# Performance work log

Hardware: AMD Instinct MI355X
Metric: run time of the kernel (lower is better)

The kernel has to match this reference:

```python
import jax, jax.numpy as jnp
import numpy as np

D_MODEL = 2048
R = 32
LN_EPS = 1e-5  # torch nn.LayerNorm default


def setup_inputs() -> dict:
    key = jax.random.key(0)
    k_x, k_wd, k_wu = jax.random.split(key, 3)
    x = jax.random.normal(k_x, (4, 4096, D_MODEL), dtype=jnp.float32)
    gamma = jnp.ones((D_MODEL,), dtype=jnp.float32)
    beta = jnp.zeros((D_MODEL,), dtype=jnp.float32)
    # down: default torch Linear init ~ U(-1/sqrt(d), 1/sqrt(d)); approximate with scaled normal
    w_down = jax.random.normal(k_wd, (D_MODEL, R), dtype=jnp.float32) / jnp.sqrt(jnp.float32(D_MODEL))
    b_down = jnp.zeros((R,), dtype=jnp.float32)
    # up: nn.init.normal_(std=0.001), bias zero
    w_up = jax.random.normal(k_wu, (R, D_MODEL), dtype=jnp.float32) * 0.001
    b_up = jnp.zeros((D_MODEL,), dtype=jnp.float32)
    return {"x": x, "gamma": gamma, "beta": beta, "w_down": w_down,
            "b_down": b_down, "w_up": w_up, "b_up": b_up}


def reference(x, gamma, beta, w_down, b_down, w_up, b_up):
    # LayerNorm over last dim
    mu = jnp.mean(x, axis=-1, keepdims=True)
    var = jnp.mean(jnp.square(x - mu), axis=-1, keepdims=True)
    h = (x - mu) * jax.lax.rsqrt(var + LN_EPS) * gamma + beta
    # down-proj -> exact GELU (torch nn.GELU default) -> up-proj -> residual
    h = jnp.einsum('bsd,dr->bsr', h, w_down) + b_down
    h = jax.nn.gelu(h, approximate=False)
    h = jnp.einsum('bsr,rd->bsd', h, w_up) + b_up
    return x + h
```

## Files before the change

### kernel.cpp

```cpp
#include <hip/hip_runtime.h>
#include <math.h>

#define D     2048
#define NR    32
#define ROWS  8
#define JP    68
#define XRW   (32 * JP)

__device__ __forceinline__ void fma4(float a, const float4& w, float4& o) {
    o.x = fmaf(a, w.x, o.x);
    o.y = fmaf(a, w.y, o.y);
    o.z = fmaf(a, w.z, o.z);
    o.w = fmaf(a, w.w, o.w);
}

__device__ __forceinline__ float wred(float v) {
    #pragma unroll
    for (int off = 32; off >= 1; off >>= 1) v += __shfl_xor(v, off);
    return v;
}

__global__ __launch_bounds__(256)
void k_prep(const float* __restrict__ wd, const float* __restrict__ gamma,
            const float* __restrict__ beta, float* __restrict__ wdp,
            float* __restrict__ c12p)
{
    __shared__ float red[4][64];
    const int tid = threadIdx.x;
    const int l = tid & 63, w = tid >> 6;
    const int j = blockIdx.x * 256 + tid;

    const float gv = gamma[j], bv = beta[j];
    float4 c1a[8], c2a[8];
    #pragma unroll
    for (int q = 0; q < 8; ++q) {
        float4 wv = *(const float4*)(wd + j * NR + q * 4);
        float4 wp = make_float4(gv * wv.x, gv * wv.y, gv * wv.z, gv * wv.w);
        *(float4*)(wdp + j * NR + q * 4) = wp;
        c1a[q] = wp;
        c2a[q] = make_float4(bv * wv.x, bv * wv.y, bv * wv.z, bv * wv.w);
    }
    #pragma unroll
    for (int q = 0; q < 8; ++q) {
        c1a[q].x = wred(c1a[q].x); c1a[q].y = wred(c1a[q].y);
        c1a[q].z = wred(c1a[q].z); c1a[q].w = wred(c1a[q].w);
        c2a[q].x = wred(c2a[q].x); c2a[q].y = wred(c2a[q].y);
        c2a[q].z = wred(c2a[q].z); c2a[q].w = wred(c2a[q].w);
    }
    if (l == 0) {
        #pragma unroll
        for (int q = 0; q < 8; ++q) {
            red[w][q * 4 + 0] = c1a[q].x; red[w][q * 4 + 1] = c1a[q].y;
            red[w][q * 4 + 2] = c1a[q].z; red[w][q * 4 + 3] = c1a[q].w;
            red[w][32 + q * 4 + 0] = c2a[q].x; red[w][32 + q * 4 + 1] = c2a[q].y;
            red[w][32 + q * 4 + 2] = c2a[q].z; red[w][32 + q * 4 + 3] = c2a[q].w;
        }
    }
    __syncthreads();
    if (tid < 64)
        c12p[blockIdx.x * 64 + tid] = red[0][tid] + red[1][tid] + red[2][tid] + red[3][tid];
}

__global__ __launch_bounds__(256, 2)
void k_fused(const float* __restrict__ x, const float* __restrict__ bd,
             const float* __restrict__ wu, const float* __restrict__ bu,
             const float* __restrict__ wdp, const float* __restrict__ c12p,
             float* __restrict__ out)
{
    __shared__ float xs[ROWS * XRW];
    __shared__ float S4[4][ROWS][NR];
    __shared__ float a_s[ROWS][NR];
    __shared__ float mu_s[ROWS], rs_s[ROWS];
    __shared__ float c1s[NR], c2s[NR], bds[NR];

    const int tid = threadIdx.x;
    const int w = tid >> 6, l = tid & 63;
    const long row0 = (long)blockIdx.x * ROWS;

    if (tid < NR) {
        float a1 = 0.f, a2 = 0.f;
        #pragma unroll
        for (int p = 0; p < 8; ++p) {
            a1 += c12p[p * 64 + tid];
            a2 += c12p[p * 64 + 32 + tid];
        }
        c1s[tid] = a1; c2s[tid] = a2; bds[tid] = bd[tid];
    }

    #pragma unroll
    for (int rp = 0; rp < 2; ++rp) {
        const int row = w * 2 + rp;
        const float* xr = x + (row0 + row) * D;
        float s = 0.f, s2 = 0.f;
        #pragma unroll
        for (int it = 0; it < 8; ++it) {
            const int j = it * 256 + l * 4;
            float4 v = *(const float4*)(xr + j);
            *(float4*)&xs[row * XRW + (j >> 6) * JP + (j & 63)] = v;
            s  += v.x + v.y + v.z + v.w;
            s2 += v.x * v.x + v.y * v.y + v.z * v.z + v.w * v.w;
        }
        #pragma unroll
        for (int off = 32; off >= 1; off >>= 1) {
            s  += __shfl_xor(s, off);
            s2 += __shfl_xor(s2, off);
        }
        if (l == 0) {
            const float mu  = s * (1.0f / D);
            const float var = s2 * (1.0f / D) - mu * mu;
            mu_s[row] = mu;
            rs_s[row] = rsqrtf(var + 1e-5f);
        }
    }
    __syncthreads();

    {
        const int rg = tid & 7, r0 = rg * 4, jo = tid >> 3;
        float4 acc[ROWS];
        #pragma unroll
        for (int m = 0; m < ROWS; ++m) acc[m] = make_float4(0.f, 0.f, 0.f, 0.f);

        const float* wp_base = wdp + (jo * 64) * NR + r0;
        #pragma unroll 4
        for (int tq = 0; tq < 16; ++tq) {
            const float4 w0 = *(const float4*)(wp_base + (tq * 4 + 0) * NR);
            const float4 w1 = *(const float4*)(wp_base + (tq * 4 + 1) * NR);
            const float4 w2 = *(const float4*)(wp_base + (tq * 4 + 2) * NR);
            const float4 w3 = *(const float4*)(wp_base + (tq * 4 + 3) * NR);
            #pragma unroll
            for (int m = 0; m < ROWS; ++m) {
                const float4 xv = *(const float4*)&xs[m * XRW + jo * JP + tq * 4];
                fma4(xv.x, w0, acc[m]);
                fma4(xv.y, w1, acc[m]);
                fma4(xv.z, w2, acc[m]);
                fma4(xv.w, w3, acc[m]);
            }
        }
        #pragma unroll
        for (int m = 0; m < ROWS; ++m) {
            #pragma unroll
            for (int off = 8; off <= 32; off <<= 1) {
                acc[m].x += __shfl_xor(acc[m].x, off);
                acc[m].y += __shfl_xor(acc[m].y, off);
                acc[m].z += __shfl_xor(acc[m].z, off);
                acc[m].w += __shfl_xor(acc[m].w, off);
            }
        }
        if (l < 8) {
            #pragma unroll
            for (int m = 0; m < ROWS; ++m)
                *(float4*)&S4[w][m][l * 4] = acc[m];
        }
    }
    __syncthreads();

    {
        const int m = tid >> 5, r = tid & 31;
        const float S = S4[0][m][r] + S4[1][m][r] + S4[2][m][r] + S4[3][m][r];
        const float y = rs_s[m] * (S - mu_s[m] * c1s[r]) + c2s[r] + bds[r];
        a_s[m][r] = 0.5f * y * (1.0f + erff(y * 0.70710678118654752f));
    }
    __syncthreads();

    #pragma unroll 1
    for (int c = 0; c < 2; ++c) {
        const int j  = c * 1024 + tid * 4;
        const int xo = (j >> 6) * JP + (j & 63);
        const float4 bv = *(const float4*)(bu + j);
        float4 o[ROWS];
        #pragma unroll
        for (int m = 0; m < ROWS; ++m) {
            const float4 xv = *(const float4*)&xs[m * XRW + xo];
            o[m] = make_float4(xv.x + bv.x, xv.y + bv.y, xv.z + bv.z, xv.w + bv.w);
        }
        #pragma unroll 4
        for (int rq = 0; rq < 8; ++rq) {
            float4 ar[ROWS];
            #pragma unroll
            for (int m = 0; m < ROWS; ++m)
                ar[m] = *(const float4*)&a_s[m][rq * 4];
            #pragma unroll
            for (int rr = 0; rr < 4; ++rr) {
                const float4 wv = *(const float4*)(wu + (rq * 4 + rr) * D + j);
                #pragma unroll
                for (int m = 0; m < ROWS; ++m) {
                    const float av = (rr == 0) ? ar[m].x : (rr == 1) ? ar[m].y
                                   : (rr == 2) ? ar[m].z : ar[m].w;
                    fma4(av, wv, o[m]);
                }
            }
        }
        #pragma unroll
        for (int m = 0; m < ROWS; ++m) {
            float* op = out + (row0 + m) * D + j;
            __builtin_nontemporal_store(o[m].x, op + 0);
            __builtin_nontemporal_store(o[m].y, op + 1);
            __builtin_nontemporal_store(o[m].z, op + 2);
            __builtin_nontemporal_store(o[m].w, op + 3);
        }
    }
}

extern "C" void kernel_launch(void* const* d_in, const int* in_sizes, int n_in,
                              void* d_out, int out_size, void* d_ws, size_t ws_size,
                              hipStream_t stream) {
    (void)n_in; (void)ws_size; (void)out_size;
    const float* x     = (const float*)d_in[0];
    const float* gamma = (const float*)d_in[1];
    const float* beta  = (const float*)d_in[2];
    const float* wd    = (const float*)d_in[3];
    const float* bd    = (const float*)d_in[4];
    const float* wu    = (const float*)d_in[5];
    const float* bu    = (const float*)d_in[6];
    float* out  = (float*)d_out;
    float* wdp  = (float*)d_ws;
    float* c12p = wdp + D * NR;

    const int nrows  = in_sizes[0] / D;
    const int blocks = nrows / ROWS;

    hipLaunchKernelGGL(k_prep,  dim3(8),      dim3(256), 0, stream, wd, gamma, beta, wdp, c12p);
    hipLaunchKernelGGL(k_fused, dim3(blocks), dim3(256), 0, stream, x, bd, wu, bu, wdp, c12p, out);
}
```

Before: 283.3 us.

## Store x tile as bf16 in LDS and reload fp32 x from global for residual

The LDS copy of the x tile is now packed as bf16 pairs, which halves shared memory per block, and launch bounds are raised to allow four blocks per CU. The down-projection dot product reads the bf16 values, while the residual add re-reads full-precision x from global memory (likely an L2 hit). This trades a second global read and bf16 rounding in the down-projection for higher occupancy. The bf16 error is scaled by the small up-projection weights, so accuracy risk is modest.

Result: slower. 305.5 us (+7.8%).

```diff
diff --git a/kernel.cpp b/kernel.cpp
--- a/kernel.cpp
+++ b/kernel.cpp
@@ -4,8 +4,15 @@
 #define D     2048
 #define NR    32
 #define ROWS  8
-#define JP    68
-#define XRW   (32 * JP)
+#define CU    34
+#define XRU   (32 * CU)
+
+__device__ __forceinline__ unsigned int f2bf(float f) {
+    unsigned int u = __float_as_uint(f);
+    return (u + 0x7FFFu + ((u >> 16) & 1u)) >> 16;
+}
+__device__ __forceinline__ float bflo(unsigned int p) { return __uint_as_float(p << 16); }
+__device__ __forceinline__ float bfhi(unsigned int p) { return __uint_as_float(p & 0xFFFF0000u); }
 
 __device__ __forceinline__ void fma4(float a, const float4& w, float4& o) {
     o.x = fmaf(a, w.x, o.x);
@@ -61,13 +68,13 @@
         c12p[blockIdx.x * 64 + tid] = red[0][tid] + red[1][tid] + red[2][tid] + red[3][tid];
 }
 
-__global__ __launch_bounds__(256, 2)
+__global__ __launch_bounds__(256, 4)
 void k_fused(const float* __restrict__ x, const float* __restrict__ bd,
              const float* __restrict__ wu, const float* __restrict__ bu,
              const float* __restrict__ wdp, const float* __restrict__ c12p,
              float* __restrict__ out)
 {
-    __shared__ float xs[ROWS * XRW];
+    __shared__ unsigned int xs[ROWS * XRU];
     __shared__ float S4[4][ROWS][NR];
     __shared__ float a_s[ROWS][NR];
     __shared__ float mu_s[ROWS], rs_s[ROWS];
@@ -96,7 +103,10 @@
         for (int it = 0; it < 8; ++it) {
             const int j = it * 256 + l * 4;
             float4 v = *(const float4*)(xr + j);
-            *(float4*)&xs[row * XRW + (j >> 6) * JP + (j & 63)] = v;
+            uint2 p;
+            p.x = f2bf(v.x) | (f2bf(v.y) << 16);
+            p.y = f2bf(v.z) | (f2bf(v.w) << 16);
+            *(uint2*)&xs[row * XRU + (j >> 6) * CU + ((j & 63) >> 1)] = p;
             s  += v.x + v.y + v.z + v.w;
             s2 += v.x * v.x + v.y * v.y + v.z * v.z + v.w * v.w;
         }
@@ -121,6 +131,7 @@
         for (int m = 0; m < ROWS; ++m) acc[m] = make_float4(0.f, 0.f, 0.f, 0.f);
 
         const float* wp_base = wdp + (jo * 64) * NR + r0;
+        const unsigned int* xb = xs + jo * CU;
         #pragma unroll 4
         for (int tq = 0; tq < 16; ++tq) {
             const float4 w0 = *(const float4*)(wp_base + (tq * 4 + 0) * NR);
@@ -129,11 +140,11 @@
             const float4 w3 = *(const float4*)(wp_base + (tq * 4 + 3) * NR);
             #pragma unroll
             for (int m = 0; m < ROWS; ++m) {
-                const float4 xv = *(const float4*)&xs[m * XRW + jo * JP + tq * 4];
-                fma4(xv.x, w0, acc[m]);
-                fma4(xv.y, w1, acc[m]);
-                fma4(xv.z, w2, acc[m]);
-                fma4(xv.w, w3, acc[m]);
+                const uint2 hp = *(const uint2*)&xb[m * XRU + tq * 2];
+                fma4(bflo(hp.x), w0, acc[m]);
+                fma4(bfhi(hp.x), w1, acc[m]);
+                fma4(bflo(hp.y), w2, acc[m]);
+                fma4(bfhi(hp.y), w3, acc[m]);
             }
         }
         #pragma unroll
@@ -164,13 +175,12 @@
 
     #pragma unroll 1
     for (int c = 0; c < 2; ++c) {
-        const int j  = c * 1024 + tid * 4;
-        const int xo = (j >> 6) * JP + (j & 63);
+        const int j = c * 1024 + tid * 4;
         const float4 bv = *(const float4*)(bu + j);
         float4 o[ROWS];
         #pragma unroll
         for (int m = 0; m < ROWS; ++m) {
-            const float4 xv = *(const float4*)&xs[m * XRW + xo];
+            const float4 xv = *(const float4*)(x + (row0 + m) * D + j);
             o[m] = make_float4(xv.x + bv.x, xv.y + bv.y, xv.z + bv.z, xv.w + bv.w);
         }
         #pragma unroll 4
```

## Use bf16 MFMA for down and up projections with swizzled LDS and pre-packed weights

Applied to the files above, without the earlier changes.

Replaces the fp32 FMA loops for both low-rank projections with 16x16x32 bf16 MFMA instructions. x is stored in LDS as bf16 with an XOR swizzle, and both weight matrices are pre-packed into the MFMA fragment layout by a prep kernel. A small extra kernel reduces the LayerNorm-folding constants. The residual pass now re-reads x from global memory instead of LDS, and bf16 rounding of the activations and weights lowers the projection precision. Shared-memory use drops, so occupancy can rise to 4 blocks per SM, but only 8 of the 16 MFMA rows are used.

Result: no change. 287.5 us (+1.5%).

```diff
diff --git a/kernel.cpp b/kernel.cpp
--- a/kernel.cpp
+++ b/kernel.cpp
@@ -4,88 +4,91 @@
 #define D     2048
 #define NR    32
 #define ROWS  8
-#define JP    68
-#define XRW   (32 * JP)
-
-__device__ __forceinline__ void fma4(float a, const float4& w, float4& o) {
-    o.x = fmaf(a, w.x, o.x);
-    o.y = fmaf(a, w.y, o.y);
-    o.z = fmaf(a, w.z, o.z);
-    o.w = fmaf(a, w.w, o.w);
-}
-
-__device__ __forceinline__ float wred(float v) {
-    #pragma unroll
-    for (int off = 32; off >= 1; off >>= 1) v += __shfl_xor(v, off);
-    return v;
-}
-
-__global__ __launch_bounds__(256)
+
+typedef short bf16x8 __attribute__((ext_vector_type(8)));
+typedef float f32x4  __attribute__((ext_vector_type(4)));
+
+__device__ __forceinline__ unsigned int f2bf(float f) {
+    unsigned int u = __float_as_uint(f);
+    return (u + 0x7FFFu + ((u >> 16) & 1u)) >> 16;
+}
+__device__ __forceinline__ unsigned int pk2(float a, float b) {
+    return f2bf(a) | (f2bf(b) << 16);
+}
+
+__global__ __launch_bounds__(64)
 void k_prep(const float* __restrict__ wd, const float* __restrict__ gamma,
-            const float* __restrict__ beta, float* __restrict__ wdp,
+            const float* __restrict__ beta, const float* __restrict__ wu,
+            unsigned int* __restrict__ wuf, unsigned int* __restrict__ wdpf,
             float* __restrict__ c12p)
 {
-    __shared__ float red[4][64];
-    const int tid = threadIdx.x;
-    const int l = tid & 63, w = tid >> 6;
-    const int j = blockIdx.x * 256 + tid;
-
-    const float gv = gamma[j], bv = beta[j];
-    float4 c1a[8], c2a[8];
-    #pragma unroll
-    for (int q = 0; q < 8; ++q) {
-        float4 wv = *(const float4*)(wd + j * NR + q * 4);
-        float4 wp = make_float4(gv * wv.x, gv * wv.y, gv * wv.z, gv * wv.w);
-        *(float4*)(wdp + j * NR + q * 4) = wp;
-        c1a[q] = wp;
-        c2a[q] = make_float4(bv * wv.x, bv * wv.y, bv * wv.z, bv * wv.w);
-    }
-    #pragma unroll
-    for (int q = 0; q < 8; ++q) {
-        c1a[q].x = wred(c1a[q].x); c1a[q].y = wred(c1a[q].y);
-        c1a[q].z = wred(c1a[q].z); c1a[q].w = wred(c1a[q].w);
-        c2a[q].x = wred(c2a[q].x); c2a[q].y = wred(c2a[q].y);
-        c2a[q].z = wred(c2a[q].z); c2a[q].w = wred(c2a[q].w);
-    }
-    if (l == 0) {
-        #pragma unroll
-        for (int q = 0; q < 8; ++q) {
-            red[w][q * 4 + 0] = c1a[q].x; red[w][q * 4 + 1] = c1a[q].y;
-            red[w][q * 4 + 2] = c1a[q].z; red[w][q * 4 + 3] = c1a[q].w;
-            red[w][32 + q * 4 + 0] = c2a[q].x; red[w][32 + q * 4 + 1] = c2a[q].y;
-            red[w][32 + q * 4 + 2] = c2a[q].z; red[w][32 + q * 4 + 3] = c2a[q].w;
-        }
-    }
-    __syncthreads();
-    if (tid < 64)
-        c12p[blockIdx.x * 64 + tid] = red[0][tid] + red[1][tid] + red[2][tid] + red[3][tid];
-}
-
-__global__ __launch_bounds__(256, 2)
+    const int l = threadIdx.x;
+    const int q = l >> 4, p = l & 15;
+    const int b = blockIdx.x;
+    if (b < 128) {
+        const int t = b;
+        float v[8];
+        #pragma unroll
+        for (int e = 0; e < 8; ++e)
+            v[e] = wu[(q * 8 + e) * D + t * 16 + p];
+        uint4 pk;
+        pk.x = pk2(v[0], v[1]); pk.y = pk2(v[2], v[3]);
+        pk.z = pk2(v[4], v[5]); pk.w = pk2(v[6], v[7]);
+        *(uint4*)&wuf[(t * 64 + l) * 4] = pk;
+    } else {
+        const int idx = b - 128;
+        const int kk = idx >> 1, n = idx & 1;
+        const int r = n * 16 + p;
+        float wv[8];
+        float c1 = 0.f, c2 = 0.f;
+        #pragma unroll
+        for (int e = 0; e < 8; ++e) {
+            const int k = kk * 32 + q * 8 + e;
+            const float wdv = wd[k * NR + r];
+            wv[e] = gamma[k] * wdv;
+            c1 += wv[e];
+            c2 += beta[k] * wdv;
+        }
+        uint4 pk;
+        pk.x = pk2(wv[0], wv[1]); pk.y = pk2(wv[2], wv[3]);
+        pk.z = pk2(wv[4], wv[5]); pk.w = pk2(wv[6], wv[7]);
+        *(uint4*)&wdpf[(idx * 64 + l) * 4] = pk;
+        c1 += __shfl_xor(c1, 16); c1 += __shfl_xor(c1, 32);
+        c2 += __shfl_xor(c2, 16); c2 += __shfl_xor(c2, 32);
+        if (q == 0) {
+            c12p[idx * 32 + p]      = c1;
+            c12p[idx * 32 + 16 + p] = c2;
+        }
+    }
+}
+
+__global__ __launch_bounds__(64)
+void k_c12(const float* __restrict__ c12p, float* __restrict__ c12)
+{
+    const int i = threadIdx.x;
+    const int half = i >> 5, r = i & 31;
+    const int n = r >> 4, rr = r & 15;
+    float s = 0.f;
+    for (int kk = 0; kk < 64; ++kk)
+        s += c12p[(kk * 2 + n) * 32 + half * 16 + rr];
+    c12[i] = s;
+}
+
+__global__ __launch_bounds__(256, 4)
 void k_fused(const float* __restrict__ x, const float* __restrict__ bd,
-             const float* __restrict__ wu, const float* __restrict__ bu,
-             const float* __restrict__ wdp, const float* __restrict__ c12p,
+             const float* __restrict__ bu, const unsigned int* __restrict__ wuf,
+             const unsigned int* __restrict__ wdpf, const float* __restrict__ c12,
              float* __restrict__ out)
 {
-    __shared__ float xs[ROWS * XRW];
-    __shared__ float S4[4][ROWS][NR];
-    __shared__ float a_s[ROWS][NR];
+    __shared__ unsigned int xs[ROWS * 1024];
+    __shared__ float Sp[4][2][16][8];
+    __shared__ unsigned short a_sh[ROWS][NR];
     __shared__ float mu_s[ROWS], rs_s[ROWS];
-    __shared__ float c1s[NR], c2s[NR], bds[NR];
 
     const int tid = threadIdx.x;
     const int w = tid >> 6, l = tid & 63;
+    const int p = l & 15, q = l >> 4;
     const long row0 = (long)blockIdx.x * ROWS;
-
-    if (tid < NR) {
-        float a1 = 0.f, a2 = 0.f;
-        #pragma unroll
-        for (int p = 0; p < 8; ++p) {
-            a1 += c12p[p * 64 + tid];
-            a2 += c12p[p * 64 + 32 + tid];
-        }
-        c1s[tid] = a1; c2s[tid] = a2; bds[tid] = bd[tid];
-    }
 
     #pragma unroll
     for (int rp = 0; rp < 2; ++rp) {
@@ -96,7 +99,11 @@
         for (int it = 0; it < 8; ++it) {
             const int j = it * 256 + l * 4;
             float4 v = *(const float4*)(xr + j);
-            *(float4*)&xs[row * XRW + (j >> 6) * JP + (j & 63)] = v;
+            uint2 pkk;
+            pkk.x = pk2(v.x, v.y);
+            pkk.y = pk2(v.z, v.w);
+            const int byte = (row * 4096 + j * 2) ^ (row << 4);
+            *(uint2*)((char*)xs + byte) = pkk;
             s  += v.x + v.y + v.z + v.w;
             s2 += v.x * v.x + v.y * v.y + v.z * v.z + v.w * v.w;
         }
@@ -115,88 +122,60 @@
     __syncthreads();
 
     {
-        const int rg = tid & 7, r0 = rg * 4, jo = tid >> 3;
-        float4 acc[ROWS];
-        #pragma unroll
-        for (int m = 0; m < ROWS; ++m) acc[m] = make_float4(0.f, 0.f, 0.f, 0.f);
-
-        const float* wp_base = wdp + (jo * 64) * NR + r0;
+        f32x4 acc0 = {0.f, 0.f, 0.f, 0.f}, acc1 = {0.f, 0.f, 0.f, 0.f};
+        const bool arow = p < ROWS;
         #pragma unroll 4
-        for (int tq = 0; tq < 16; ++tq) {
-            const float4 w0 = *(const float4*)(wp_base + (tq * 4 + 0) * NR);
-            const float4 w1 = *(const float4*)(wp_base + (tq * 4 + 1) * NR);
-            const float4 w2 = *(const float4*)(wp_base + (tq * 4 + 2) * NR);
-            const float4 w3 = *(const float4*)(wp_base + (tq * 4 + 3) * NR);
-            #pragma unroll
-            for (int m = 0; m < ROWS; ++m) {
-                const float4 xv = *(const float4*)&xs[m * XRW + jo * JP + tq * 4];
-                fma4(xv.x, w0, acc[m]);
-                fma4(xv.y, w1, acc[m]);
-                fma4(xv.z, w2, acc[m]);
-                fma4(xv.w, w3, acc[m]);
+        for (int t = 0; t < 16; ++t) {
+            bf16x8 af = {0, 0, 0, 0, 0, 0, 0, 0};
+            if (arow) {
+                const int byte = (p * 4096 + (w * 512 + t * 32) * 2 + q * 16) ^ (p << 4);
+                af = *(const bf16x8*)((const char*)xs + byte);
             }
-        }
-        #pragma unroll
-        for (int m = 0; m < ROWS; ++m) {
-            #pragma unroll
-            for (int off = 8; off <= 32; off <<= 1) {
-                acc[m].x += __shfl_xor(acc[m].x, off);
-                acc[m].y += __shfl_xor(acc[m].y, off);
-                acc[m].z += __shfl_xor(acc[m].z, off);
-                acc[m].w += __shfl_xor(acc[m].w, off);
-            }
-        }
-        if (l < 8) {
-            #pragma unroll
-            for (int m = 0; m < ROWS; ++m)
-                *(float4*)&S4[w][m][l * 4] = acc[m];
+            const int base = (w * 16 + t) * 512 + l * 4;
+            const bf16x8 b0 = *(const bf16x8*)&wdpf[base];
+            const bf16x8 b1 = *(const bf16x8*)&wdpf[base + 256];
+            acc0 = __builtin_amdgcn_mfma_f32_16x16x32_bf16(af, b0, acc0, 0, 0, 0);
+            acc1 = __builtin_amdgcn_mfma_f32_16x16x32_bf16(af, b1, acc1, 0, 0, 0);
+        }
+        if (l < 32) {
+            *(f32x4*)&Sp[w][0][p][(q & 1) * 4] = acc0;
+            *(f32x4*)&Sp[w][1][p][(q & 1) * 4] = acc1;
         }
     }
     __syncthreads();
 
     {
         const int m = tid >> 5, r = tid & 31;
-        const float S = S4[0][m][r] + S4[1][m][r] + S4[2][m][r] + S4[3][m][r];
-        const float y = rs_s[m] * (S - mu_s[m] * c1s[r]) + c2s[r] + bds[r];
-        a_s[m][r] = 0.5f * y * (1.0f + erff(y * 0.70710678118654752f));
+        const int n = r >> 4, rr = r & 15;
+        const float S = Sp[0][n][rr][m] + Sp[1][n][rr][m]
+                      + Sp[2][n][rr][m] + Sp[3][n][rr][m];
+        const float y = rs_s[m] * (S - mu_s[m] * c12[r]) + c12[32 + r] + bd[r];
+        const float a = 0.5f * y * (1.0f + erff(y * 0.70710678118654752f));
+        a_sh[m][r] = (unsigned short)f2bf(a);
     }
     __syncthreads();
 
-    #pragma unroll 1
-    for (int c = 0; c < 2; ++c) {
-        const int j  = c * 1024 + tid * 4;
-        const int xo = (j >> 6) * JP + (j & 63);
-        const float4 bv = *(const float4*)(bu + j);
-        float4 o[ROWS];
-        #pragma unroll
-        for (int m = 0; m < ROWS; ++m) {
-            const float4 xv = *(const float4*)&xs[m * XRW + xo];
-            o[m] = make_float4(xv.x + bv.x, xv.y + bv.y, xv.z + bv.z, xv.w + bv.w);
-        }
+    {
+        bf16x8 afc = {0, 0, 0, 0, 0, 0, 0, 0};
+        if (p < ROWS) afc = *(const bf16x8*)((const char*)a_sh + p * 64 + q * 16);
+        const bool act = p < ROWS;
+        const long xbase = (row0 + p) * D;
+        const f32x4 z = {0.f, 0.f, 0.f, 0.f};
         #pragma unroll 4
-        for (int rq = 0; rq < 8; ++rq) {
-            float4 ar[ROWS];
-            #pragma unroll
-            for (int m = 0; m < ROWS; ++m)
-                ar[m] = *(const float4*)&a_s[m][rq * 4];
-            #pragma unroll
-            for (int rr = 0; rr < 4; ++rr) {
-                const float4 wv = *(const float4*)(wu + (rq * 4 + rr) * D + j);
-                #pragma unroll
-                for (int m = 0; m < ROWS; ++m) {
-                    const float av = (rr == 0) ? ar[m].x : (rr == 1) ? ar[m].y
-                                   : (rr == 2) ? ar[m].z : ar[m].w;
-                    fma4(av, wv, o[m]);
-                }
+        for (int t = 0; t < 32; ++t) {
+            const int j0 = w * 512 + t * 16;
+            const bf16x8 bw = *(const bf16x8*)&wuf[(j0 >> 4) * 256 + l * 4];
+            f32x4 dd = __builtin_amdgcn_mfma_f32_16x16x32_bf16(bw, afc, z, 0, 0, 0);
+            if (act) {
+                const int jj = j0 + q * 4;
+                const float4 xv = *(const float4*)(x + xbase + jj);
+                const float4 bv = *(const float4*)(bu + jj);
+                float* op = out + xbase + jj;
+                __builtin_nontemporal_store(xv.x + bv.x + dd[0], op + 0);
+                __builtin_nontemporal_store(xv.y + bv.y + dd[1], op + 1);
+                __builtin_nontemporal_store(xv.z + bv.z + dd[2], op + 2);
+                __builtin_nontemporal_store(xv.w + bv.w + dd[3], op + 3);
             }
-        }
-        #pragma unroll
-        for (int m = 0; m < ROWS; ++m) {
-            float* op = out + (row0 + m) * D + j;
-            __builtin_nontemporal_store(o[m].x, op + 0);
-            __builtin_nontemporal_store(o[m].y, op + 1);
-            __builtin_nontemporal_store(o[m].z, op + 2);
-            __builtin_nontemporal_store(o[m].w, op + 3);
         }
     }
 }
@@ -212,13 +191,19 @@
     const float* bd    = (const float*)d_in[4];
     const float* wu    = (const float*)d_in[5];
     const float* bu    = (const float*)d_in[6];
-    float* out  = (float*)d_out;
-    float* wdp  = (float*)d_ws;
-    float* c12p = wdp + D * NR;
+    float* out = (float*)d_out;
+
+    unsigned int* wuf  = (unsigned int*)d_ws;
+    unsigned int* wdpf = wuf + 32768;
+    float* c12p = (float*)(wdpf + 32768);
+    float* c12  = c12p + 4096;
 
     const int nrows  = in_sizes[0] / D;
     const int blocks = nrows / ROWS;
 
-    hipLaunchKernelGGL(k_prep,  dim3(8),      dim3(256), 0, stream, wd, gamma, beta, wdp, c12p);
-    hipLaunchKernelGGL(k_fused, dim3(blocks), dim3(256), 0, stream, x, bd, wu, bu, wdp, c12p, out);
-}
+    hipLaunchKernelGGL(k_prep,  dim3(256),    dim3(64),  0, stream,
+                       wd, gamma, beta, wu, wuf, wdpf, c12p);
+    hipLaunchKernelGGL(k_c12,   dim3(1),      dim3(64),  0, stream, c12p, c12);
+    hipLaunchKernelGGL(k_fused, dim3(blocks), dim3(256), 0, stream,
+                       x, bd, bu, wuf, wdpf, c12, out);
+}
```
